# Kernel tuning notes

Measured on AMD Instinct MI355X. Metric: run time of the kernel, lower is better.

## Reference

```python
import jax, jax.numpy as jnp
import numpy as np


def setup_inputs() -> dict:
    key = jax.random.key(0)
    k1, k2 = jax.random.split(key)
    B, C, N = 32, 512, 4096
    x = jax.random.normal(k1, (B, C, N), dtype=jnp.float32)
    gamma = jax.random.normal(k2, (1,), dtype=jnp.float32)
    return {"x": x, "gamma": gamma}


def reference(x, gamma):
    # x: [B, C, N]. Channel attention: energy = x @ x^T -> [B, C, C]
    energy = jnp.einsum('bcn,bdn->bcd', x, x)
    # inverted score: rowmax - energy, then softmax over last dim
    energy_new = jnp.max(energy, axis=-1, keepdims=True) - energy
    attention = jax.nn.softmax(energy_new, axis=-1)  # [B, C, C]
    out = jnp.einsum('bcd,bdn->bcn', attention, x)
    return gamma * out + x
```

## Files before the change

kernel.cpp:

```cpp
#include <hip/hip_runtime.h>
#include <stdint.h>
#include <stddef.h>

#define NB 32
#define NC 512
#define NN 4096
#define NSPLIT 4
#define KCH (NN / NSPLIT)

typedef _Float16 h4_t __attribute__((ext_vector_type(4)));
typedef _Float16 h8_t __attribute__((ext_vector_type(8)));
typedef float    f4_t __attribute__((ext_vector_type(4)));

__device__ __forceinline__ void gload16(const _Float16* g, _Float16* l) {
    __builtin_amdgcn_global_load_lds(
        (const __attribute__((address_space(1))) void*)g,
        (__attribute__((address_space(3))) void*)l, 16, 0, 0);
}


__global__ __launch_bounds__(256) void cast_transpose(
    const float* __restrict__ x, _Float16* __restrict__ Xh,
    _Float16* __restrict__ Xl, _Float16* __restrict__ Xt)
{
    __shared__ __attribute__((aligned(16))) _Float16 tile[64 * 66];
    const int b = blockIdx.z, c0 = blockIdx.y * 64, n0 = blockIdx.x * 64;
    const int t = threadIdx.x;
    const int lr = t >> 4;
    const int lc = (t & 15) * 4;
    const size_t xbase = (size_t)b * NC * NN;

#pragma unroll
    for (int p = 0; p < 4; ++p) {
        const int r = p * 16 + lr;
        const size_t off = xbase + (size_t)(c0 + r) * NN + (n0 + lc);
        const float4 v = *(const float4*)(x + off);
        const _Float16 h0 = (_Float16)v.x, h1 = (_Float16)v.y;
        const _Float16 h2 = (_Float16)v.z, h3 = (_Float16)v.w;
        h4_t hv = {h0, h1, h2, h3};
        *(h4_t*)(Xh + off) = hv;
        h4_t lv = {(_Float16)(v.x - (float)h0), (_Float16)(v.y - (float)h1),
                   (_Float16)(v.z - (float)h2), (_Float16)(v.w - (float)h3)};
        *(h4_t*)(Xl + off) = lv;
        tile[r * 66 + lc + 0] = h0;
        tile[r * 66 + lc + 1] = h1;
        tile[r * 66 + lc + 2] = h2;
        tile[r * 66 + lc + 3] = h3;
    }
    __syncthreads();
    const size_t tbase = (size_t)b * NN * NC;
#pragma unroll
    for (int p = 0; p < 4; ++p) {
        const int rn = p * 16 + lr;
        h4_t w;
        w[0] = tile[(lc + 0) * 66 + rn];
        w[1] = tile[(lc + 1) * 66 + rn];
        w[2] = tile[(lc + 2) * 66 + rn];
        w[3] = tile[(lc + 3) * 66 + rn];
        *(h4_t*)(Xt + tbase + (size_t)(n0 + rn) * NC + (c0 + lc)) = w;
    }
}

__global__ __launch_bounds__(256) void cast_hl(
    const float* __restrict__ x, _Float16* __restrict__ Xh,
    _Float16* __restrict__ Xl)
{
    const size_t total = (size_t)NB * NC * NN / 4;
    for (size_t i = (size_t)blockIdx.x * 256 + threadIdx.x; i < total;
         i += (size_t)gridDim.x * 256) {
        const float4 v = ((const float4*)x)[i];
        const _Float16 h0 = (_Float16)v.x, h1 = (_Float16)v.y;
        const _Float16 h2 = (_Float16)v.z, h3 = (_Float16)v.w;
        h4_t hv = {h0, h1, h2, h3};
        h4_t lv = {(_Float16)(v.x - (float)h0), (_Float16)(v.y - (float)h1),
                   (_Float16)(v.z - (float)h2), (_Float16)(v.w - (float)h3)};
        ((h4_t*)Xh)[i] = hv;
        ((h4_t*)Xl)[i] = lv;
    }
}

__global__ __launch_bounds__(256, 4) void gemm1_energy(
    const _Float16* __restrict__ Xh, const _Float16* __restrict__ Xl,
    float* __restrict__ part)
{
    __shared__ __attribute__((aligned(16))) _Float16 sAh[128 * 32];
    __shared__ __attribute__((aligned(16))) _Float16 sBh[128 * 32];
    __shared__ __attribute__((aligned(16))) _Float16 sAl[128 * 32];
    __shared__ __attribute__((aligned(16))) _Float16 sBl[128 * 32];

    const int flat = blockIdx.x;
    const int xcd  = flat & 7;
    const int slot = flat >> 3;
    const int grp  = xcd + 8 * (slot / 10);
    const int mem  = slot % 10;
    const int b    = grp >> 2;
    const int s    = grp & (NSPLIT - 1);

    const int ti = (int)((sqrtf(8.0f * (float)mem + 1.0f) - 1.0f) * 0.5f);
    const int tj = mem - ((ti * (ti + 1)) >> 1);
    const bool diag = (ti == tj);

    const int t = threadIdx.x;
    const int wave = t >> 6, lane = t & 63;
    const int srow = t >> 2;
    const int scol = (((t & 3) ^ ((t >> 3) & 3)) * 8);

    const size_t xb = (size_t)b * NC * NN + (size_t)s * KCH;
    const _Float16* gAh = Xh + xb + (size_t)(ti * 128 + srow) * NN + scol;
    const _Float16* gBh = Xh + xb + (size_t)(tj * 128 + srow) * NN + scol;
    const _Float16* gAl = Xl + xb + (size_t)(ti * 128 + srow) * NN + scol;
    const _Float16* gBl = Xl + xb + (size_t)(tj * 128 + srow) * NN + scol;

    const int wr = wave >> 1, wc = wave & 1;
    const int fr = lane & 15, fko = (lane >> 4) * 8;
    const int hi4 = (lane >> 4) * 4;
    const int fsw = fko ^ (((fr >> 1) & 3) << 3);

    const _Float16* rBh = diag ? sAh : sBh;
    const _Float16* rBl = diag ? sAl : sBl;

    f4_t acc[4][4];
#pragma unroll
    for (int m = 0; m < 4; ++m)
#pragma unroll
        for (int n = 0; n < 4; ++n) acc[m][n] = (f4_t){0.f, 0.f, 0.f, 0.f};

    for (int k0 = 0; k0 < KCH; k0 += 32) {
        gload16(gAh + k0,                   sAh + wave * 512);
        gload16(gAh + k0 + 64 * (size_t)NN, sAh + 2048 + wave * 512);
        gload16(gAl + k0,                   sAl + wave * 512);
        gload16(gAl + k0 + 64 * (size_t)NN, sAl + 2048 + wave * 512);
        if (!diag) {
            gload16(gBh + k0,                   sBh + wave * 512);
            gload16(gBh + k0 + 64 * (size_t)NN, sBh + 2048 + wave * 512);
            gload16(gBl + k0,                   sBl + wave * 512);
            gload16(gBl + k0 + 64 * (size_t)NN, sBl + 2048 + wave * 512);
        }
        __syncthreads();

        h8_t ah[4], bh[4], al[4], bl[4];
#pragma unroll
        for (int m = 0; m < 4; ++m) {
            ah[m] = *(const h8_t*)(sAh + (wr * 64 + m * 16 + fr) * 32 + fsw);
            bh[m] = *(const h8_t*)(rBh + (wc * 64 + m * 16 + fr) * 32 + fsw);
            al[m] = *(const h8_t*)(sAl + (wr * 64 + m * 16 + fr) * 32 + fsw);
            bl[m] = *(const h8_t*)(rBl + (wc * 64 + m * 16 + fr) * 32 + fsw);
        }
#pragma unroll
        for (int m = 0; m < 4; ++m)
#pragma unroll
            for (int nf = 0; nf < 4; ++nf) {
                acc[nf][m] = __builtin_amdgcn_mfma_f32_16x16x32_f16(bh[nf], ah[m], acc[nf][m], 0, 0, 0);
                acc[nf][m] = __builtin_amdgcn_mfma_f32_16x16x32_f16(bl[nf], ah[m], acc[nf][m], 0, 0, 0);
                acc[nf][m] = __builtin_amdgcn_mfma_f32_16x16x32_f16(bh[nf], al[m], acc[nf][m], 0, 0, 0);
            }
        __syncthreads();
    }

    float* pb = part + ((size_t)s * NB + b) * (NC * NC);
#pragma unroll
    for (int m = 0; m < 4; ++m) {
        const int i = ti * 128 + wr * 64 + m * 16 + fr;
#pragma unroll
        for (int nf = 0; nf < 4; ++nf) {
            const int jjb = tj * 128 + wc * 64 + nf * 16 + hi4;
            *(f4_t*)(pb + (size_t)i * NC + jjb) = acc[nf][m];
            if (!diag) {
#pragma unroll
                for (int j = 0; j < 4; ++j)
                    pb[(size_t)(jjb + j) * NC + i] = acc[nf][m][j];
            }
        }
    }
}

__global__ __launch_bounds__(256) void softmax_inv(
    const float* __restrict__ part, _Float16* __restrict__ attn)
{
    const int row = blockIdx.x * 4 + (threadIdx.x >> 6);
    const int lane = threadIdx.x & 63;
    const size_t roff = (size_t)row * NC;

    float4 a0 = {0.f, 0.f, 0.f, 0.f}, a1 = {0.f, 0.f, 0.f, 0.f};
#pragma unroll
    for (int s = 0; s < NSPLIT; ++s) {
        const float4* p = (const float4*)(part + (size_t)s * NB * NC * NC + roff);
        const float4 v0 = p[lane], v1 = p[64 + lane];
        a0.x += v0.x; a0.y += v0.y; a0.z += v0.z; a0.w += v0.w;
        a1.x += v1.x; a1.y += v1.y; a1.z += v1.z; a1.w += v1.w;
    }

    float mn = fminf(fminf(fminf(a0.x, a0.y), fminf(a0.z, a0.w)),
                     fminf(fminf(a1.x, a1.y), fminf(a1.z, a1.w)));
#pragma unroll
    for (int off = 32; off; off >>= 1) mn = fminf(mn, __shfl_xor(mn, off));

    const float w0 = __expf(mn - a0.x), w1 = __expf(mn - a0.y);
    const float w2 = __expf(mn - a0.z), w3 = __expf(mn - a0.w);
    const float w4 = __expf(mn - a1.x), w5 = __expf(mn - a1.y);
    const float w6 = __expf(mn - a1.z), w7 = __expf(mn - a1.w);
    float sum = ((w0 + w1) + (w2 + w3)) + ((w4 + w5) + (w6 + w7));
#pragma unroll
    for (int off = 32; off; off >>= 1) sum += __shfl_xor(sum, off);
    const float inv = 1.0f / sum;

    h4_t o0 = {(_Float16)(w0 * inv), (_Float16)(w1 * inv),
               (_Float16)(w2 * inv), (_Float16)(w3 * inv)};
    h4_t o1 = {(_Float16)(w4 * inv), (_Float16)(w5 * inv),
               (_Float16)(w6 * inv), (_Float16)(w7 * inv)};
    ((h4_t*)(attn + roff))[lane] = o0;
    ((h4_t*)(attn + roff))[64 + lane] = o1;
}

__global__ __launch_bounds__(256) void transpose_h(
    const _Float16* __restrict__ Xh, _Float16* __restrict__ Xt)
{
    __shared__ __attribute__((aligned(16))) _Float16 tile[64 * 66];
    const int b = blockIdx.z, c0 = blockIdx.y * 64, n0 = blockIdx.x * 64;
    const int t = threadIdx.x;
    const int lr = t >> 4;
    const int lc = (t & 15) * 4;
    const size_t hbase = (size_t)b * NC * NN;

#pragma unroll
    for (int p = 0; p < 4; ++p) {
        const int r = p * 16 + lr;
        const h4_t v = *(const h4_t*)(Xh + hbase + (size_t)(c0 + r) * NN + (n0 + lc));
        tile[r * 66 + lc + 0] = v[0];
        tile[r * 66 + lc + 1] = v[1];
        tile[r * 66 + lc + 2] = v[2];
        tile[r * 66 + lc + 3] = v[3];
    }
    __syncthreads();
    const size_t tbase = (size_t)b * NN * NC;
#pragma unroll
    for (int p = 0; p < 4; ++p) {
        const int rn = p * 16 + lr;
        h4_t w;
        w[0] = tile[(lc + 0) * 66 + rn];
        w[1] = tile[(lc + 1) * 66 + rn];
        w[2] = tile[(lc + 2) * 66 + rn];
        w[3] = tile[(lc + 3) * 66 + rn];
        *(h4_t*)(Xt + tbase + (size_t)(n0 + rn) * NC + (c0 + lc)) = w;
    }
}

__global__ __launch_bounds__(256) void gemm2_out(
    const _Float16* __restrict__ attn, const _Float16* __restrict__ Xt,
    const _Float16* __restrict__ Xh, const float* __restrict__ gammap,
    float* __restrict__ out)
{
    __shared__ __attribute__((aligned(16))) _Float16 sA[3][128 * 32];
    __shared__ __attribute__((aligned(16))) _Float16 sB[3][128 * 32];

    const int flat = blockIdx.x;
    const int xcd  = flat & 7;
    const int slot = flat >> 3;
    const int b    = xcd + 8 * (slot >> 7);
    const int memb = slot & 127;
    const int brow = (memb & 3) * 128;
    const int bcol = (memb >> 2) * 128;

    const int t = threadIdx.x;
    const int wave = t >> 6, lane = t & 63;
    const int wr = wave >> 1, wc = wave & 1;
    const int fr = lane & 15, fq = lane >> 4;
    const int hi4 = fq * 4;

    const int rr = t >> 2;
    const int sck = (((t & 3) ^ ((rr >> 1) & 3)) * 8);
    const _Float16* gA = attn + (size_t)b * NC * NC + (size_t)brow * NC;
    const _Float16* gB = Xt   + (size_t)b * NN * NC + (size_t)bcol * NC;

    f4_t acc[4][4];
#pragma unroll
    for (int m = 0; m < 4; ++m)
#pragma unroll
        for (int n = 0; n < 4; ++n) acc[m][n] = (f4_t){0.f, 0.f, 0.f, 0.f};

#define STG2(buf, k0)                                                         \
    {                                                                         \
        gload16(gA + (size_t)rr * NC + (k0) + sck,        &sA[buf][0] + t * 8); \
        gload16(gA + (size_t)(64 + rr) * NC + (k0) + sck, &sA[buf][0] + 2048 + t * 8); \
        gload16(gB + (size_t)rr * NC + (k0) + sck,        &sB[buf][0] + t * 8); \
        gload16(gB + (size_t)(64 + rr) * NC + (k0) + sck, &sB[buf][0] + 2048 + t * 8); \
    }

    STG2(0, 0);
    STG2(1, 32);

#pragma unroll
    for (int it = 0; it < 16; ++it) {
        if (it < 15) {
            asm volatile("s_waitcnt vmcnt(4)" ::: "memory");
        } else {
            asm volatile("s_waitcnt vmcnt(0)" ::: "memory");
        }
        __builtin_amdgcn_s_barrier();
        if (it + 2 < 16) STG2((it + 2) % 3, (it + 2) * 32);

        const _Float16* cA = &sA[it % 3][0];
        const _Float16* cB = &sB[it % 3][0];
        h8_t a_[4], b_[4];
#pragma unroll
        for (int m = 0; m < 4; ++m) {
            const int ar = wr * 64 + m * 16 + fr;
            const int br = wc * 64 + m * 16 + fr;
            a_[m] = *(const h8_t*)(cA + ar * 32 + ((fq ^ ((ar >> 1) & 3)) * 8));
            b_[m] = *(const h8_t*)(cB + br * 32 + ((fq ^ ((br >> 1) & 3)) * 8));
        }
#pragma unroll
        for (int m = 0; m < 4; ++m)
#pragma unroll
            for (int nf = 0; nf < 4; ++nf)
                acc[nf][m] = __builtin_amdgcn_mfma_f32_16x16x32_f16(
                    b_[nf], a_[m], acc[nf][m], 0, 0, 0);
    }
#undef STG2

    const float g = gammap[0];
    const _Float16* xb = Xh + (size_t)b * NC * NN;
    float* ob = out + (size_t)b * NC * NN;
#pragma unroll
    for (int m = 0; m < 4; ++m) {
        const int c_ = brow + wr * 64 + m * 16 + fr;
#pragma unroll
        for (int nf = 0; nf < 4; ++nf) {
            const int n_ = bcol + wc * 64 + nf * 16 + hi4;
            const size_t off = (size_t)c_ * NN + n_;
            const h4_t xv = *(const h4_t*)(xb + off);
            f4_t o;
#pragma unroll
            for (int j = 0; j < 4; ++j)
                o[j] = g * acc[nf][m][j] + (float)xv[j];
            *(f4_t*)(ob + off) = o;
        }
    }
}

extern "C" void kernel_launch(void* const* d_in, const int* in_sizes, int n_in,
                              void* d_out, int out_size, void* d_ws, size_t ws_size,
                              hipStream_t stream)
{
    const float* x     = (const float*)d_in[0];
    const float* gamma = (const float*)d_in[1];
    float* out = (float*)d_out;
    char* ws = (char*)d_ws;

    if (ws_size >= 553648128ull) {
        _Float16* Xh   = (_Float16*)(ws);
        _Float16* Xl   = (_Float16*)(ws + 134217728ull);
        _Float16* Xt   = (_Float16*)(ws + 268435456ull);
        _Float16* attn = (_Float16*)(ws + 402653184ull);
        float*    part = (float*)   (ws + 419430400ull);

        cast_transpose<<<dim3(NN / 64, NC / 64, NB), 256, 0, stream>>>(x, Xh, Xl, Xt);
        gemm1_energy<<<dim3(10 * NSPLIT * NB), 256, 0, stream>>>(Xh, Xl, part);
        softmax_inv<<<dim3(NB * NC / 4), 256, 0, stream>>>(part, attn);
        gemm2_out<<<dim3(4096), 256, 0, stream>>>(attn, Xt, Xh, gamma, out);
    } else {
        _Float16* Xh   = (_Float16*)(ws);
        _Float16* XlXt = (_Float16*)(ws + 134217728ull);
        _Float16* attn = (_Float16*)(ws + 268435456ull);
        float*    part = (float*)   (ws + 285212672ull);

        cast_hl<<<dim3(2048), 256, 0, stream>>>(x, Xh, XlXt);
        gemm1_energy<<<dim3(10 * NSPLIT * NB), 256, 0, stream>>>(Xh, XlXt, part);
        softmax_inv<<<dim3(NB * NC / 4), 256, 0, stream>>>(part, attn);
        transpose_h<<<dim3(NN / 64, NC / 64, NB), 256, 0, stream>>>(Xh, XlXt);
        gemm2_out<<<dim3(4096), 256, 0, stream>>>(attn, XlXt, Xh, gamma, out);
    }
}
```

Measured before the change: 465.3 us.

## Enlarge GEMM tiles to 256x256 with 512-thread blocks and deeper pipelining

Both GEMMs move from 128x128 tiles with 256 threads to 256x256 tiles with 512 threads, each wave computing a 128x64 sub-tile. This raises arithmetic intensity and cuts redundant global and LDS traffic. The energy GEMM now uses symmetric 2x2 block tiling (3 tiles per batch), gains double-buffered LDS staging, and takes a runtime split-K count (8 when the workspace allows). The output GEMM goes from a 3-stage to a 4-stage LDS ring with adjusted vmcnt waits. The larger LDS footprint (about 128KB per block) limits each CU to one resident block, and the extra split-K partials add reduction traffic in the softmax.

```diff
diff --git a/kernel.cpp b/kernel.cpp
--- a/kernel.cpp
+++ b/kernel.cpp
@@ -5,8 +5,6 @@
 #define NB 32
 #define NC 512
 #define NN 4096
-#define NSPLIT 4
-#define KCH (NN / NSPLIT)
 
 typedef _Float16 h4_t __attribute__((ext_vector_type(4)));
 typedef _Float16 h8_t __attribute__((ext_vector_type(8)));
@@ -79,91 +77,108 @@
     }
 }
 
-__global__ __launch_bounds__(256, 4) void gemm1_energy(
+__global__ __launch_bounds__(512, 2) void gemm1_energy(
     const _Float16* __restrict__ Xh, const _Float16* __restrict__ Xl,
-    float* __restrict__ part)
-{
-    __shared__ __attribute__((aligned(16))) _Float16 sAh[128 * 32];
-    __shared__ __attribute__((aligned(16))) _Float16 sBh[128 * 32];
-    __shared__ __attribute__((aligned(16))) _Float16 sAl[128 * 32];
-    __shared__ __attribute__((aligned(16))) _Float16 sBl[128 * 32];
+    float* __restrict__ part, int kch, int nsplit)
+{
+    __shared__ __attribute__((aligned(16))) _Float16 sAh[2][256 * 32];
+    __shared__ __attribute__((aligned(16))) _Float16 sAl[2][256 * 32];
+    __shared__ __attribute__((aligned(16))) _Float16 sBh[2][256 * 32];
+    __shared__ __attribute__((aligned(16))) _Float16 sBl[2][256 * 32];
 
     const int flat = blockIdx.x;
-    const int xcd  = flat & 7;
-    const int slot = flat >> 3;
-    const int grp  = xcd + 8 * (slot / 10);
-    const int mem  = slot % 10;
-    const int b    = grp >> 2;
-    const int s    = grp & (NSPLIT - 1);
-
-    const int ti = (int)((sqrtf(8.0f * (float)mem + 1.0f) - 1.0f) * 0.5f);
-    const int tj = mem - ((ti * (ti + 1)) >> 1);
-    const bool diag = (ti == tj);
+    const int cpx  = 12 * nsplit;
+    const int swz  = (flat & 7) * cpx + (flat >> 3);
+    const int per_b = 3 * nsplit;
+    const int b   = swz / per_b;
+    const int rem = swz % per_b;
+    const int s   = rem / 3;
+    const int mem = rem % 3;
+    const int ti  = (mem >= 1) ? 1 : 0;
+    const int tj  = (mem == 2) ? 1 : 0;
+    const bool diag = (mem != 1);
 
     const int t = threadIdx.x;
     const int wave = t >> 6, lane = t & 63;
-    const int srow = t >> 2;
-    const int scol = (((t & 3) ^ ((t >> 3) & 3)) * 8);
-
-    const size_t xb = (size_t)b * NC * NN + (size_t)s * KCH;
-    const _Float16* gAh = Xh + xb + (size_t)(ti * 128 + srow) * NN + scol;
-    const _Float16* gBh = Xh + xb + (size_t)(tj * 128 + srow) * NN + scol;
-    const _Float16* gAl = Xl + xb + (size_t)(ti * 128 + srow) * NN + scol;
-    const _Float16* gBl = Xl + xb + (size_t)(tj * 128 + srow) * NN + scol;
-
-    const int wr = wave >> 1, wc = wave & 1;
-    const int fr = lane & 15, fko = (lane >> 4) * 8;
-    const int hi4 = (lane >> 4) * 4;
-    const int fsw = fko ^ (((fr >> 1) & 3) << 3);
-
-    const _Float16* rBh = diag ? sAh : sBh;
-    const _Float16* rBl = diag ? sAl : sBl;
-
-    f4_t acc[4][4];
-#pragma unroll
-    for (int m = 0; m < 4; ++m)
-#pragma unroll
-        for (int n = 0; n < 4; ++n) acc[m][n] = (f4_t){0.f, 0.f, 0.f, 0.f};
-
-    for (int k0 = 0; k0 < KCH; k0 += 32) {
-        gload16(gAh + k0,                   sAh + wave * 512);
-        gload16(gAh + k0 + 64 * (size_t)NN, sAh + 2048 + wave * 512);
-        gload16(gAl + k0,                   sAl + wave * 512);
-        gload16(gAl + k0 + 64 * (size_t)NN, sAl + 2048 + wave * 512);
-        if (!diag) {
-            gload16(gBh + k0,                   sBh + wave * 512);
-            gload16(gBh + k0 + 64 * (size_t)NN, sBh + 2048 + wave * 512);
-            gload16(gBl + k0,                   sBl + wave * 512);
-            gload16(gBl + k0 + 64 * (size_t)NN, sBl + 2048 + wave * 512);
+    const int wr = wave >> 2, wc = wave & 3;
+    const int fr = lane & 15, fq = lane >> 4;
+    const int hi4 = fq * 4;
+
+    const int rr  = t >> 2;
+    const int sck = (((t & 3) ^ ((t >> 3) & 3)) * 8);
+
+    const size_t xb = (size_t)b * NC * NN + (size_t)s * kch;
+    const _Float16* gAh = Xh + xb + (size_t)(ti * 256 + rr) * NN + sck;
+    const _Float16* gAl = Xl + xb + (size_t)(ti * 256 + rr) * NN + sck;
+    const _Float16* gBh = Xh + xb + (size_t)(tj * 256 + rr) * NN + sck;
+    const _Float16* gBl = Xl + xb + (size_t)(tj * 256 + rr) * NN + sck;
+    const size_t P = (size_t)128 * NN;
+
+    f4_t acc[4][8];
+#pragma unroll
+    for (int nf = 0; nf < 4; ++nf)
+#pragma unroll
+        for (int m = 0; m < 8; ++m) acc[nf][m] = (f4_t){0.f, 0.f, 0.f, 0.f};
+
+#define STG1(buf, k0)                                                        \
+    {                                                                        \
+        gload16(gAh + (k0),     &sAh[buf][0] + t * 8);                       \
+        gload16(gAh + (k0) + P, &sAh[buf][0] + 4096 + t * 8);                \
+        gload16(gAl + (k0),     &sAl[buf][0] + t * 8);                       \
+        gload16(gAl + (k0) + P, &sAl[buf][0] + 4096 + t * 8);                \
+        if (!diag) {                                                         \
+            gload16(gBh + (k0),     &sBh[buf][0] + t * 8);                   \
+            gload16(gBh + (k0) + P, &sBh[buf][0] + 4096 + t * 8);            \
+            gload16(gBl + (k0),     &sBl[buf][0] + t * 8);                   \
+            gload16(gBl + (k0) + P, &sBl[buf][0] + 4096 + t * 8);            \
+        }                                                                    \
+    }
+
+    STG1(0, 0);
+    __syncthreads();
+
+    const int nIter = kch >> 5;
+    for (int it = 0; it < nIter; ++it) {
+        const int cur = it & 1;
+        if (it + 1 < nIter) STG1(cur ^ 1, (it + 1) * 32);
+
+        const _Float16* cAh = &sAh[cur][0];
+        const _Float16* cAl = &sAl[cur][0];
+        const _Float16* cBh = diag ? cAh : &sBh[cur][0];
+        const _Float16* cBl = diag ? cAl : &sBl[cur][0];
+
+        h8_t bh_[4], bl_[4];
+#pragma unroll
+        for (int nf = 0; nf < 4; ++nf) {
+            const int br = wc * 64 + nf * 16 + fr;
+            const int so = (fq ^ ((br >> 1) & 3)) * 8;
+            bh_[nf] = *(const h8_t*)(cBh + br * 32 + so);
+            bl_[nf] = *(const h8_t*)(cBl + br * 32 + so);
+        }
+#pragma unroll
+        for (int m = 0; m < 8; ++m) {
+            const int ar = wr * 128 + m * 16 + fr;
+            const int so = (fq ^ ((ar >> 1) & 3)) * 8;
+            const h8_t ah = *(const h8_t*)(cAh + ar * 32 + so);
+            const h8_t al = *(const h8_t*)(cAl + ar * 32 + so);
+#pragma unroll
+            for (int nf = 0; nf < 4; ++nf) {
+                acc[nf][m] = __builtin_amdgcn_mfma_f32_16x16x32_f16(bh_[nf], ah, acc[nf][m], 0, 0, 0);
+                acc[nf][m] = __builtin_amdgcn_mfma_f32_16x16x32_f16(bl_[nf], ah, acc[nf][m], 0, 0, 0);
+                acc[nf][m] = __builtin_amdgcn_mfma_f32_16x16x32_f16(bh_[nf], al, acc[nf][m], 0, 0, 0);
+            }
         }
         __syncthreads();
-
-        h8_t ah[4], bh[4], al[4], bl[4];
-#pragma unroll
-        for (int m = 0; m < 4; ++m) {
-            ah[m] = *(const h8_t*)(sAh + (wr * 64 + m * 16 + fr) * 32 + fsw);
-            bh[m] = *(const h8_t*)(rBh + (wc * 64 + m * 16 + fr) * 32 + fsw);
-            al[m] = *(const h8_t*)(sAl + (wr * 64 + m * 16 + fr) * 32 + fsw);
-            bl[m] = *(const h8_t*)(rBl + (wc * 64 + m * 16 + fr) * 32 + fsw);
-        }
-#pragma unroll
-        for (int m = 0; m < 4; ++m)
-#pragma unroll
-            for (int nf = 0; nf < 4; ++nf) {
-                acc[nf][m] = __builtin_amdgcn_mfma_f32_16x16x32_f16(bh[nf], ah[m], acc[nf][m], 0, 0, 0);
-                acc[nf][m] = __builtin_amdgcn_mfma_f32_16x16x32_f16(bl[nf], ah[m], acc[nf][m], 0, 0, 0);
-                acc[nf][m] = __builtin_amdgcn_mfma_f32_16x16x32_f16(bh[nf], al[m], acc[nf][m], 0, 0, 0);
-            }
-        __syncthreads();
-    }
+    }
+#undef STG1
 
     float* pb = part + ((size_t)s * NB + b) * (NC * NC);
 #pragma unroll
-    for (int m = 0; m < 4; ++m) {
-        const int i = ti * 128 + wr * 64 + m * 16 + fr;
+    for (int m = 0; m < 8; ++m) {
+        const int i = ti * 256 + wr * 128 + m * 16 + fr;
 #pragma unroll
         for (int nf = 0; nf < 4; ++nf) {
-            const int jjb = tj * 128 + wc * 64 + nf * 16 + hi4;
+            const int jjb = tj * 256 + wc * 64 + nf * 16 + hi4;
             *(f4_t*)(pb + (size_t)i * NC + jjb) = acc[nf][m];
             if (!diag) {
 #pragma unroll
@@ -175,15 +190,14 @@
 }
 
 __global__ __launch_bounds__(256) void softmax_inv(
-    const float* __restrict__ part, _Float16* __restrict__ attn)
+    const float* __restrict__ part, _Float16* __restrict__ attn, int nsplit)
 {
     const int row = blockIdx.x * 4 + (threadIdx.x >> 6);
     const int lane = threadIdx.x & 63;
     const size_t roff = (size_t)row * NC;
 
     float4 a0 = {0.f, 0.f, 0.f, 0.f}, a1 = {0.f, 0.f, 0.f, 0.f};
-#pragma unroll
-    for (int s = 0; s < NSPLIT; ++s) {
+    for (int s = 0; s < nsplit; ++s) {
         const float4* p = (const float4*)(part + (size_t)s * NB * NC * NC + roff);
         const float4 v0 = p[lane], v1 = p[64 + lane];
         a0.x += v0.x; a0.y += v0.y; a0.z += v0.z; a0.w += v0.w;
@@ -245,76 +259,76 @@
     }
 }
 
-__global__ __launch_bounds__(256) void gemm2_out(
+__global__ __launch_bounds__(512, 2) void gemm2_out(
     const _Float16* __restrict__ attn, const _Float16* __restrict__ Xt,
     const _Float16* __restrict__ Xh, const float* __restrict__ gammap,
     float* __restrict__ out)
 {
-    __shared__ __attribute__((aligned(16))) _Float16 sA[3][128 * 32];
-    __shared__ __attribute__((aligned(16))) _Float16 sB[3][128 * 32];
+    __shared__ __attribute__((aligned(16))) _Float16 sA[4][256 * 32];
+    __shared__ __attribute__((aligned(16))) _Float16 sB[4][256 * 32];
 
     const int flat = blockIdx.x;
-    const int xcd  = flat & 7;
-    const int slot = flat >> 3;
-    const int b    = xcd + 8 * (slot >> 7);
-    const int memb = slot & 127;
-    const int brow = (memb & 3) * 128;
-    const int bcol = (memb >> 2) * 128;
+    const int swz  = (flat & 7) * 128 + (flat >> 3);
+    const int b    = swz >> 5;
+    const int memb = swz & 31;
+    const int brow = (memb & 1) * 256;
+    const int bcol = (memb >> 1) * 256;
 
     const int t = threadIdx.x;
     const int wave = t >> 6, lane = t & 63;
-    const int wr = wave >> 1, wc = wave & 1;
+    const int wr = wave >> 2, wc = wave & 3;
     const int fr = lane & 15, fq = lane >> 4;
     const int hi4 = fq * 4;
 
-    const int rr = t >> 2;
-    const int sck = (((t & 3) ^ ((rr >> 1) & 3)) * 8);
-    const _Float16* gA = attn + (size_t)b * NC * NC + (size_t)brow * NC;
-    const _Float16* gB = Xt   + (size_t)b * NN * NC + (size_t)bcol * NC;
-
-    f4_t acc[4][4];
-#pragma unroll
-    for (int m = 0; m < 4; ++m)
-#pragma unroll
-        for (int n = 0; n < 4; ++n) acc[m][n] = (f4_t){0.f, 0.f, 0.f, 0.f};
-
-#define STG2(buf, k0)                                                         \
-    {                                                                         \
-        gload16(gA + (size_t)rr * NC + (k0) + sck,        &sA[buf][0] + t * 8); \
-        gload16(gA + (size_t)(64 + rr) * NC + (k0) + sck, &sA[buf][0] + 2048 + t * 8); \
-        gload16(gB + (size_t)rr * NC + (k0) + sck,        &sB[buf][0] + t * 8); \
-        gload16(gB + (size_t)(64 + rr) * NC + (k0) + sck, &sB[buf][0] + 2048 + t * 8); \
+    const int rr  = t >> 2;
+    const int sck = (((t & 3) ^ ((t >> 3) & 3)) * 8);
+    const _Float16* gA = attn + (size_t)b * NC * NC + (size_t)(brow + rr) * NC + sck;
+    const _Float16* gB = Xt   + (size_t)b * NN * NC + (size_t)(bcol + rr) * NC + sck;
+    const size_t P = (size_t)128 * NC;
+
+    f4_t acc[4][8];
+#pragma unroll
+    for (int nf = 0; nf < 4; ++nf)
+#pragma unroll
+        for (int m = 0; m < 8; ++m) acc[nf][m] = (f4_t){0.f, 0.f, 0.f, 0.f};
+
+#define STG2(buf, k0)                                                        \
+    {                                                                        \
+        gload16(gA + (k0),     &sA[buf][0] + t * 8);                         \
+        gload16(gA + (k0) + P, &sA[buf][0] + 4096 + t * 8);                  \
+        gload16(gB + (k0),     &sB[buf][0] + t * 8);                         \
+        gload16(gB + (k0) + P, &sB[buf][0] + 4096 + t * 8);                  \
     }
 
     STG2(0, 0);
     STG2(1, 32);
+    STG2(2, 64);
 
 #pragma unroll
     for (int it = 0; it < 16; ++it) {
-        if (it < 15) {
-            asm volatile("s_waitcnt vmcnt(4)" ::: "memory");
-        } else {
-            asm volatile("s_waitcnt vmcnt(0)" ::: "memory");
-        }
+        if (it <= 13)       asm volatile("s_waitcnt vmcnt(8)" ::: "memory");
+        else if (it == 14)  asm volatile("s_waitcnt vmcnt(4)" ::: "memory");
+        else                asm volatile("s_waitcnt vmcnt(0)" ::: "memory");
         __builtin_amdgcn_s_barrier();
-        if (it + 2 < 16) STG2((it + 2) % 3, (it + 2) * 32);
-
-        const _Float16* cA = &sA[it % 3][0];
-        const _Float16* cB = &sB[it % 3][0];
-        h8_t a_[4], b_[4];
-#pragma unroll
-        for (int m = 0; m < 4; ++m) {
-            const int ar = wr * 64 + m * 16 + fr;
-            const int br = wc * 64 + m * 16 + fr;
-            a_[m] = *(const h8_t*)(cA + ar * 32 + ((fq ^ ((ar >> 1) & 3)) * 8));
-            b_[m] = *(const h8_t*)(cB + br * 32 + ((fq ^ ((br >> 1) & 3)) * 8));
-        }
-#pragma unroll
-        for (int m = 0; m < 4; ++m)
+        if (it <= 12) STG2((it + 3) & 3, (it + 3) * 32);
+
+        const _Float16* cA = &sA[it & 3][0];
+        const _Float16* cB = &sB[it & 3][0];
+        h8_t b_[4];
+#pragma unroll
+        for (int nf = 0; nf < 4; ++nf) {
+            const int br = wc * 64 + nf * 16 + fr;
+            b_[nf] = *(const h8_t*)(cB + br * 32 + ((fq ^ ((br >> 1) & 3)) * 8));
+        }
+#pragma unroll
+        for (int m = 0; m < 8; ++m) {
+            const int ar = wr * 128 + m * 16 + fr;
+            const h8_t a = *(const h8_t*)(cA + ar * 32 + ((fq ^ ((ar >> 1) & 3)) * 8));
 #pragma unroll
             for (int nf = 0; nf < 4; ++nf)
                 acc[nf][m] = __builtin_amdgcn_mfma_f32_16x16x32_f16(
-                    b_[nf], a_[m], acc[nf][m], 0, 0, 0);
+                    b_[nf], a, acc[nf][m], 0, 0, 0);
+        }
     }
 #undef STG2
 
@@ -322,8 +336,8 @@
     const _Float16* xb = Xh + (size_t)b * NC * NN;
     float* ob = out + (size_t)b * NC * NN;
 #pragma unroll
-    for (int m = 0; m < 4; ++m) {
-        const int c_ = brow + wr * 64 + m * 16 + fr;
+    for (int m = 0; m < 8; ++m) {
+        const int c_ = brow + wr * 128 + m * 16 + fr;
 #pragma unroll
         for (int nf = 0; nf < 4; ++nf) {
             const int n_ = bcol + wc * 64 + nf * 16 + hi4;
@@ -353,11 +367,13 @@
         _Float16* Xt   = (_Float16*)(ws + 268435456ull);
         _Float16* attn = (_Float16*)(ws + 402653184ull);
         float*    part = (float*)   (ws + 419430400ull);
+        const int nsplit = (ws_size >= 687865856ull) ? 8 : 4;
+        const int kch = NN / nsplit;
 
         cast_transpose<<<dim3(NN / 64, NC / 64, NB), 256, 0, stream>>>(x, Xh, Xl, Xt);
-        gemm1_energy<<<dim3(10 * NSPLIT * NB), 256, 0, stream>>>(Xh, Xl, part);
-        softmax_inv<<<dim3(NB * NC / 4), 256, 0, stream>>>(part, attn);
-        gemm2_out<<<dim3(4096), 256, 0, stream>>>(attn, Xt, Xh, gamma, out);
+        gemm1_energy<<<dim3(3 * nsplit * NB), 512, 0, stream>>>(Xh, Xl, part, kch, nsplit);
+        softmax_inv<<<dim3(NB * NC / 4), 256, 0, stream>>>(part, attn, nsplit);
+        gemm2_out<<<dim3(1024), 512, 0, stream>>>(attn, Xt, Xh, gamma, out);
     } else {
         _Float16* Xh   = (_Float16*)(ws);
         _Float16* XlXt = (_Float16*)(ws + 134217728ull);
@@ -365,9 +381,9 @@
         float*    part = (float*)   (ws + 285212672ull);
 
         cast_hl<<<dim3(2048), 256, 0, stream>>>(x, Xh, XlXt);
-        gemm1_energy<<<dim3(10 * NSPLIT * NB), 256, 0, stream>>>(Xh, XlXt, part);
-        softmax_inv<<<dim3(NB * NC / 4), 256, 0, stream>>>(part, attn);
+        gemm1_energy<<<dim3(3 * 4 * NB), 512, 0, stream>>>(Xh, XlXt, part, NN / 4, 4);
+        softmax_inv<<<dim3(NB * NC / 4), 256, 0, stream>>>(part, attn, 4);
         transpose_h<<<dim3(NN / 64, NC / 64, NB), 256, 0, stream>>>(Xh, XlXt);
-        gemm2_out<<<dim3(4096), 256, 0, stream>>>(attn, XlXt, Xh, gamma, out);
-    }
-}
+        gemm2_out<<<dim3(1024), 512, 0, stream>>>(attn, XlXt, Xh, gamma, out);
+    }
+}
```

Result: slower. 492.1 us (+5.8%).

## Enlarge gemm2 tile to 256x256 with 512 threads and 4-stage LDS pipeline

Applied to the files above, without the earlier changes.

The output GEMM now uses 256x256 tiles computed by 8 waves (512 threads) instead of 128x128 tiles with 4 waves. Each wave handles a 128x64 sub-tile, and the K loop gains a fourth shared-memory buffer so loads run three stages ahead. The block-to-XCD swizzle is rewritten for the new 1024-block grid. The aim is more operand reuse per byte loaded and deeper latency hiding, at the cost of more LDS (128KB per block), higher register pressure and fewer blocks in the grid.

```diff
diff --git a/kernel.cpp b/kernel.cpp
--- a/kernel.cpp
+++ b/kernel.cpp
@@ -245,76 +245,76 @@
     }
 }
 
-__global__ __launch_bounds__(256) void gemm2_out(
+__global__ __launch_bounds__(512, 2) void gemm2_out(
     const _Float16* __restrict__ attn, const _Float16* __restrict__ Xt,
     const _Float16* __restrict__ Xh, const float* __restrict__ gammap,
     float* __restrict__ out)
 {
-    __shared__ __attribute__((aligned(16))) _Float16 sA[3][128 * 32];
-    __shared__ __attribute__((aligned(16))) _Float16 sB[3][128 * 32];
+    __shared__ __attribute__((aligned(16))) _Float16 sA[4][256 * 32];
+    __shared__ __attribute__((aligned(16))) _Float16 sB[4][256 * 32];
 
     const int flat = blockIdx.x;
-    const int xcd  = flat & 7;
-    const int slot = flat >> 3;
-    const int b    = xcd + 8 * (slot >> 7);
-    const int memb = slot & 127;
-    const int brow = (memb & 3) * 128;
-    const int bcol = (memb >> 2) * 128;
+    const int swz  = (flat & 7) * 128 + (flat >> 3);
+    const int b    = swz >> 5;
+    const int memb = swz & 31;
+    const int brow = (memb & 1) * 256;
+    const int bcol = (memb >> 1) * 256;
 
     const int t = threadIdx.x;
     const int wave = t >> 6, lane = t & 63;
-    const int wr = wave >> 1, wc = wave & 1;
+    const int wr = wave >> 2, wc = wave & 3;
     const int fr = lane & 15, fq = lane >> 4;
     const int hi4 = fq * 4;
 
-    const int rr = t >> 2;
-    const int sck = (((t & 3) ^ ((rr >> 1) & 3)) * 8);
-    const _Float16* gA = attn + (size_t)b * NC * NC + (size_t)brow * NC;
-    const _Float16* gB = Xt   + (size_t)b * NN * NC + (size_t)bcol * NC;
-
-    f4_t acc[4][4];
-#pragma unroll
-    for (int m = 0; m < 4; ++m)
-#pragma unroll
-        for (int n = 0; n < 4; ++n) acc[m][n] = (f4_t){0.f, 0.f, 0.f, 0.f};
-
-#define STG2(buf, k0)                                                         \
-    {                                                                         \
-        gload16(gA + (size_t)rr * NC + (k0) + sck,        &sA[buf][0] + t * 8); \
-        gload16(gA + (size_t)(64 + rr) * NC + (k0) + sck, &sA[buf][0] + 2048 + t * 8); \
-        gload16(gB + (size_t)rr * NC + (k0) + sck,        &sB[buf][0] + t * 8); \
-        gload16(gB + (size_t)(64 + rr) * NC + (k0) + sck, &sB[buf][0] + 2048 + t * 8); \
+    const int rr  = t >> 2;
+    const int sck = (((t & 3) ^ ((t >> 3) & 3)) * 8);
+    const _Float16* gA = attn + (size_t)b * NC * NC + (size_t)(brow + rr) * NC + sck;
+    const _Float16* gB = Xt   + (size_t)b * NN * NC + (size_t)(bcol + rr) * NC + sck;
+    const size_t P = (size_t)128 * NC;
+
+    f4_t acc[4][8];
+#pragma unroll
+    for (int nf = 0; nf < 4; ++nf)
+#pragma unroll
+        for (int m = 0; m < 8; ++m) acc[nf][m] = (f4_t){0.f, 0.f, 0.f, 0.f};
+
+#define STG2(buf, k0)                                                        \
+    {                                                                        \
+        gload16(gA + (k0),     &sA[buf][0] + t * 8);                         \
+        gload16(gA + (k0) + P, &sA[buf][0] + 4096 + t * 8);                  \
+        gload16(gB + (k0),     &sB[buf][0] + t * 8);                         \
+        gload16(gB + (k0) + P, &sB[buf][0] + 4096 + t * 8);                  \
     }
 
     STG2(0, 0);
     STG2(1, 32);
+    STG2(2, 64);
 
 #pragma unroll
     for (int it = 0; it < 16; ++it) {
-        if (it < 15) {
-            asm volatile("s_waitcnt vmcnt(4)" ::: "memory");
-        } else {
-            asm volatile("s_waitcnt vmcnt(0)" ::: "memory");
-        }
+        if (it <= 13)       asm volatile("s_waitcnt vmcnt(8)" ::: "memory");
+        else if (it == 14)  asm volatile("s_waitcnt vmcnt(4)" ::: "memory");
+        else                asm volatile("s_waitcnt vmcnt(0)" ::: "memory");
         __builtin_amdgcn_s_barrier();
-        if (it + 2 < 16) STG2((it + 2) % 3, (it + 2) * 32);
-
-        const _Float16* cA = &sA[it % 3][0];
-        const _Float16* cB = &sB[it % 3][0];
-        h8_t a_[4], b_[4];
-#pragma unroll
-        for (int m = 0; m < 4; ++m) {
-            const int ar = wr * 64 + m * 16 + fr;
-            const int br = wc * 64 + m * 16 + fr;
-            a_[m] = *(const h8_t*)(cA + ar * 32 + ((fq ^ ((ar >> 1) & 3)) * 8));
-            b_[m] = *(const h8_t*)(cB + br * 32 + ((fq ^ ((br >> 1) & 3)) * 8));
-        }
-#pragma unroll
-        for (int m = 0; m < 4; ++m)
+        if (it <= 12) STG2((it + 3) & 3, (it + 3) * 32);
+
+        const _Float16* cA = &sA[it & 3][0];
+        const _Float16* cB = &sB[it & 3][0];
+        h8_t b_[4];
+#pragma unroll
+        for (int nf = 0; nf < 4; ++nf) {
+            const int br = wc * 64 + nf * 16 + fr;
+            b_[nf] = *(const h8_t*)(cB + br * 32 + ((fq ^ ((br >> 1) & 3)) * 8));
+        }
+#pragma unroll
+        for (int m = 0; m < 8; ++m) {
+            const int ar = wr * 128 + m * 16 + fr;
+            const h8_t a = *(const h8_t*)(cA + ar * 32 + ((fq ^ ((ar >> 1) & 3)) * 8));
 #pragma unroll
             for (int nf = 0; nf < 4; ++nf)
                 acc[nf][m] = __builtin_amdgcn_mfma_f32_16x16x32_f16(
-                    b_[nf], a_[m], acc[nf][m], 0, 0, 0);
+                    b_[nf], a, acc[nf][m], 0, 0, 0);
+        }
     }
 #undef STG2
 
@@ -322,8 +322,8 @@
     const _Float16* xb = Xh + (size_t)b * NC * NN;
     float* ob = out + (size_t)b * NC * NN;
 #pragma unroll
-    for (int m = 0; m < 4; ++m) {
-        const int c_ = brow + wr * 64 + m * 16 + fr;
+    for (int m = 0; m < 8; ++m) {
+        const int c_ = brow + wr * 128 + m * 16 + fr;
 #pragma unroll
         for (int nf = 0; nf < 4; ++nf) {
             const int n_ = bcol + wc * 64 + nf * 16 + hi4;
@@ -357,7 +357,7 @@
         cast_transpose<<<dim3(NN / 64, NC / 64, NB), 256, 0, stream>>>(x, Xh, Xl, Xt);
         gemm1_energy<<<dim3(10 * NSPLIT * NB), 256, 0, stream>>>(Xh, Xl, part);
         softmax_inv<<<dim3(NB * NC / 4), 256, 0, stream>>>(part, attn);
-        gemm2_out<<<dim3(4096), 256, 0, stream>>>(attn, Xt, Xh, gamma, out);
+        gemm2_out<<<dim3(1024), 512, 0, stream>>>(attn, Xt, Xh, gamma, out);
     } else {
         _Float16* Xh   = (_Float16*)(ws);
         _Float16* XlXt = (_Float16*)(ws + 134217728ull);
@@ -368,6 +368,6 @@
         gemm1_energy<<<dim3(10 * NSPLIT * NB), 256, 0, stream>>>(Xh, XlXt, part);
         softmax_inv<<<dim3(NB * NC / 4), 256, 0, stream>>>(part, attn);
         transpose_h<<<dim3(NN / 64, NC / 64, NB), 256, 0, stream>>>(Xh, XlXt);
-        gemm2_out<<<dim3(4096), 256, 0, stream>>>(attn, XlXt, Xh, gamma, out);
-    }
-}
+        gemm2_out<<<dim3(1024), 512, 0, stream>>>(attn, XlXt, Xh, gamma, out);
+    }
+}
```

Result: faster. 438.6 us (-5.7%).
